# Optimization experiments

Measured on AMD Instinct MI355X. Metric: run time of the kernel, lower is better.

## Reference

```python
import jax, jax.numpy as jnp
import numpy as np

N_U, N_P, E = 200000, 50000, 500000
D_U, D_P, H, OUT = 100, 50, 128, 1
BN_EPS = 1e-5


def _lin(k, dout, din):
    s = 1.0 / np.sqrt(din)
    kw, kb = jax.random.split(k)
    W = jax.random.uniform(kw, (dout, din), jnp.float32, -s, s)
    b = jax.random.uniform(kb, (dout,), jnp.float32, -s, s)
    return W, b


def setup_inputs() -> dict:
    key = jax.random.key(0)
    ks = jax.random.split(key, 12)
    x_u = jax.random.normal(ks[0], (N_U, D_U), jnp.float32)
    x_p = jax.random.normal(ks[1], (N_P, D_P), jnp.float32)
    src = jax.random.randint(ks[2], (E,), 0, N_U, jnp.int64) if jax.config.jax_enable_x64 else jax.random.randint(ks[2], (E,), 0, N_U)
    dst = jax.random.randint(ks[3], (E,), N_U, N_U + N_P)
    edge_index = jnp.stack([src, dst]).astype(jnp.int32)
    W_u, b_u = _lin(ks[4], H, D_U)
    W_p, b_p = _lin(ks[5], H, D_P)
    W1l, b1l = _lin(ks[6], H, H)   # SAGEConv lin_l (aggregated neighbors, carries bias)
    W1r, _ = _lin(ks[7], H, H)     # SAGEConv lin_r (root, no bias)
    W2l, b2l = _lin(ks[8], H, H)
    W2r, _ = _lin(ks[9], H, H)
    W_out, b_out = _lin(ks[10], OUT, H)
    return dict(x_u=x_u, x_p=x_p, edge_index=edge_index,
                W_u=W_u, b_u=b_u, W_p=W_p, b_p=b_p,
                W1l=W1l, b1l=b1l, W1r=W1r,
                g1=jnp.ones((H,), jnp.float32), be1=jnp.zeros((H,), jnp.float32),
                W2l=W2l, b2l=b2l, W2r=W2r,
                g2=jnp.ones((H,), jnp.float32), be2=jnp.zeros((H,), jnp.float32),
                W_out=W_out, b_out=b_out)


def reference(x_u, x_p, edge_index, W_u, b_u, W_p, b_p,
              W1l, b1l, W1r, g1, be1, W2l, b2l, W2r, g2, be2,
              W_out, b_out):
    N = x_u.shape[0] + x_p.shape[0]
    # input projections + relu, then concat users/products -> [N, H]
    x = jnp.concatenate([jax.nn.relu(x_u @ W_u.T + b_u),
                         jax.nn.relu(x_p @ W_p.T + b_p)], axis=0)
    # to_undirected: add reversed edges (bipartite => no duplicates)
    src = jnp.concatenate([edge_index[0], edge_index[1]])
    dst = jnp.concatenate([edge_index[1], edge_index[0]])
    deg = jnp.maximum(jax.ops.segment_sum(jnp.ones_like(dst, jnp.float32), dst, num_segments=N), 1.0)

    def sage(h, Wl, bl, Wr):
        # mean aggregation of neighbor features, scatter by dst
        mean = jax.ops.segment_sum(h[src], dst, num_segments=N) / deg[:, None]
        return mean @ Wl.T + bl + h @ Wr.T

    def bn(h, g, b):
        m = h.mean(0)
        v = h.var(0)  # biased variance, as used for normalization in torch BN
        return (h - m) * jax.lax.rsqrt(v + BN_EPS) * g + b

    h1 = jax.nn.relu(bn(sage(x, W1l, b1l, W1r), g1, be1))   # dropout = identity (eval)
    h2 = jax.nn.relu(bn(sage(h1, W2l, b2l, W2r), g2, be2)) + x
    return h2[: x_u.shape[0]] @ W_out.T + b_out
```

## Files before the change

kernel.cpp:

```cpp
#include <hip/hip_runtime.h>
#include <hip/hip_bf16.h>
#include <cstdint>
#include <cstddef>

#define NT   250000
#define NUU  200000
#define NPP  50000
#define EG   500000
#define E2   1000000
#define HD   128
#define NBLK_SCAN 977

#define X_OFF     0ull
#define R1_OFF    64000000ull
#define R2_OFF    128000000ull
#define CNT_OFF   179200000ull
#define SPART_OFF 180200000ull
#define SS_OFF    180265536ull
#define RPTR_OFF  180267584ull
#define BSUM_OFF  181267588ull
#define BMAT_OFF  181271504ull
#define COL_OFF   181451728ull
#define WS_NEED   185451728ull

typedef __hip_bfloat16 bf16;
typedef __attribute__((ext_vector_type(8))) short short8v;
typedef __attribute__((ext_vector_type(4))) float f32x4;

__device__ inline float bflo(unsigned u) { return __builtin_bit_cast(float, u << 16); }
__device__ inline float bfhi(unsigned u) { return __builtin_bit_cast(float, u & 0xffff0000u); }
__device__ inline float b2f(short s) { return __builtin_bit_cast(float, ((unsigned)(unsigned short)s) << 16); }
__device__ inline unsigned short f2bf(float f) { return __builtin_bit_cast(unsigned short, __float2bfloat16(f)); }

__global__ __launch_bounds__(256) void k_zero(int* __restrict__ p, int n) {
    for (int i = blockIdx.x * 256 + threadIdx.x; i < n; i += gridDim.x * 256) p[i] = 0;
}

__global__ __launch_bounds__(256) void k_count(const int* __restrict__ ei, int* __restrict__ cnt) {
    for (int e = blockIdx.x * 256 + threadIdx.x; e < E2; e += gridDim.x * 256) {
        int d = (e < EG) ? ei[e + EG] : ei[e - EG];
        atomicAdd(&cnt[d], 1);
    }
}

__global__ __launch_bounds__(256) void k_scan1(const int* __restrict__ cnt, int* __restrict__ bsum) {
    __shared__ int lds[256];
    int i = blockIdx.x * 256 + threadIdx.x;
    int v = (i < NT) ? cnt[i] : 0;
    lds[threadIdx.x] = v; __syncthreads();
    for (int s = 128; s > 0; s >>= 1) {
        if (threadIdx.x < s) lds[threadIdx.x] += lds[threadIdx.x + s];
        __syncthreads();
    }
    if (threadIdx.x == 0) bsum[blockIdx.x] = lds[0];
}

__global__ __launch_bounds__(1024) void k_scan2(int* __restrict__ bsum) {
    __shared__ int lds[1024];
    int i = threadIdx.x;
    int v = (i < NBLK_SCAN) ? bsum[i] : 0;
    lds[i] = v; __syncthreads();
    for (int off = 1; off < 1024; off <<= 1) {
        int t = (i >= off) ? lds[i - off] : 0;
        __syncthreads();
        lds[i] += t;
        __syncthreads();
    }
    if (i < NBLK_SCAN) bsum[i] = lds[i] - v;
}

__global__ __launch_bounds__(256) void k_scan3(const int* __restrict__ cnt, const int* __restrict__ bsum,
                                               int* __restrict__ rp) {
    __shared__ int lds[256];
    int i = blockIdx.x * 256 + threadIdx.x;
    int v = (i < NT) ? cnt[i] : 0;
    lds[threadIdx.x] = v; __syncthreads();
    for (int off = 1; off < 256; off <<= 1) {
        int t = (threadIdx.x >= off) ? lds[threadIdx.x - off] : 0;
        __syncthreads();
        lds[threadIdx.x] += t;
        __syncthreads();
    }
    if (i < NT) rp[i] = bsum[blockIdx.x] + lds[threadIdx.x] - v;
    if (i == 0 && blockIdx.x == 0) rp[NT] = E2;
}

__global__ __launch_bounds__(256) void k_fill(const int* __restrict__ ei, const int* __restrict__ rp,
                                              int* __restrict__ fill, int* __restrict__ col) {
    for (int e = blockIdx.x * 256 + threadIdx.x; e < E2; e += gridDim.x * 256) {
        int s = ei[e];
        int d = (e < EG) ? ei[e + EG] : ei[e - EG];
        int slot = rp[d] + atomicAdd(&fill[d], 1);
        col[slot] = s;
    }
}

__global__ __launch_bounds__(256) void k_wcvt(const float* __restrict__ W1l, const float* __restrict__ W1r,
                                              const float* __restrict__ W2l, const float* __restrict__ W2r,
                                              const float* __restrict__ Wu, const float* __restrict__ Wp,
                                              bf16* __restrict__ B) {
    int i = blockIdx.x * 256 + threadIdx.x;
    if (i < 65536) {
        int layer = i >> 15, rem = i & 32767, o = rem >> 8, k = rem & 255;
        const float* W = layer ? ((k < 128) ? W2l : W2r) : ((k < 128) ? W1l : W1r);
        B[i] = __float2bfloat16(W[o * 128 + (k & 127)]);
    } else if (i < 81920) {
        int rem = i - 65536, o = rem >> 7, k = rem & 127;
        B[i] = __float2bfloat16((k < 100) ? Wu[o * 100 + k] : 0.f);
    } else if (i < 90112) {
        int rem = i - 81920, o = rem >> 6, k = rem & 63;
        B[i] = __float2bfloat16((k < 50) ? Wp[o * 50 + k] : 0.f);
    }
}

template<int DIN, int KPAD>
__global__ __launch_bounds__(256) void k_projm(const float* __restrict__ in, const bf16* __restrict__ Bp,
                                               const float* __restrict__ bias, bf16* __restrict__ outp,
                                               int nrows, int rowbase) {
    const int lane = threadIdx.x & 63;
    const int wid = threadIdx.x >> 6;
    const int wr = wid >> 1, wc = wid & 1;
    const int r15 = lane & 15, l4 = lane >> 4;
    const int tb = blockIdx.x * 128;
    constexpr int NKS = KPAD / 32;

    f32x4 acc[4][4] = {};
#pragma unroll
    for (int ks = 0; ks < NKS; ks++) {
        int kk = ks * 32 + l4 * 8;
        short8v a[4], b[4];
#pragma unroll
        for (int m = 0; m < 4; m++) {
            int r = tb + wr * 64 + m * 16 + r15;
            if (r > nrows - 1) r = nrows - 1;
            const float* src = in + (size_t)r * DIN + kk;
            short8v v;
            if constexpr (DIN >= 32 * (1) && true) {
                if (ks * 32 + 32 <= DIN) {
                    const float2* s2 = (const float2*)src;
                    float2 f0 = s2[0], f1 = s2[1], f2 = s2[2], f3 = s2[3];
                    v[0] = (short)f2bf(f0.x); v[1] = (short)f2bf(f0.y);
                    v[2] = (short)f2bf(f1.x); v[3] = (short)f2bf(f1.y);
                    v[4] = (short)f2bf(f2.x); v[5] = (short)f2bf(f2.y);
                    v[6] = (short)f2bf(f3.x); v[7] = (short)f2bf(f3.y);
                } else {
#pragma unroll
                    for (int j = 0; j < 8; j++) {
                        float f = (kk + j < DIN) ? src[j] : 0.f;
                        v[j] = (short)f2bf(f);
                    }
                }
            }
            a[m] = v;
        }
#pragma unroll
        for (int n = 0; n < 4; n++) {
            int c = wc * 64 + n * 16 + r15;
            b[n] = *(const short8v*)(Bp + (size_t)c * KPAD + kk);
        }
#pragma unroll
        for (int m = 0; m < 4; m++)
#pragma unroll
            for (int n = 0; n < 4; n++)
                acc[m][n] = __builtin_amdgcn_mfma_f32_16x16x32_bf16(a[m], b[n], acc[m][n], 0, 0, 0);
    }
    float bcol[4];
#pragma unroll
    for (int n = 0; n < 4; n++) bcol[n] = bias[wc * 64 + n * 16 + r15];
#pragma unroll
    for (int m = 0; m < 4; m++)
#pragma unroll
        for (int n = 0; n < 4; n++)
#pragma unroll
            for (int g = 0; g < 4; g++) {
                int row = tb + wr * 64 + m * 16 + l4 * 4 + g;
                if (row < nrows) {
                    float v = fmaxf(acc[m][n][g] + bcol[n], 0.f);
                    outp[(size_t)(rowbase + row) * HD + wc * 64 + n * 16 + r15] = __float2bfloat16(v);
                }
            }
}

template<bool NORM>
__global__ __launch_bounds__(256) void k_gemm(const bf16* __restrict__ hin, const float* __restrict__ ssv,
                                              const int* __restrict__ rp, const int* __restrict__ col,
                                              const bf16* __restrict__ Bmat, const float* __restrict__ blv,
                                              bf16* __restrict__ outp, float* __restrict__ spart,
                                              int store_n) {
    __shared__ unsigned int mrow[8192];
    const int tid = threadIdx.x;
    const int lane = tid & 63;
    const int wid = tid >> 6;
    const int g16 = lane >> 4, l16 = lane & 15;
    const int tb = blockIdx.x * 128;
    const int wnb = wid * 32;

    float sv[8], tv[8];
    if (NORM) {
        int f0 = l16 * 8;
#pragma unroll
        for (int j = 0; j < 8; j++) { sv[j] = ssv[f0 + j]; tv[j] = ssv[HD + f0 + j]; }
    }

    int rpv = 0;
    if (lane <= 32) {
        int idx = tb + wnb + lane;
        rpv = rp[min(idx, NT)];
    }

    for (int t = 0; t < 8; t++) {
        int nl = wnb + t * 4 + g16;
        int node = tb + nl;
        int s0 = __shfl(rpv, t * 4 + g16);
        int s1 = __shfl(rpv, t * 4 + g16 + 1);
        if (node >= NT) { s0 = 0; s1 = 0; }
        float a[8] = {0.f, 0.f, 0.f, 0.f, 0.f, 0.f, 0.f, 0.f};
        for (int p = s0; p < s1; p += 4) {
            int c0 = col[p];
            int c1 = col[min(p + 1, s1 - 1)];
            int c2 = col[min(p + 2, s1 - 1)];
            int c3 = col[min(p + 3, s1 - 1)];
            short8v u0 = *(const short8v*)(hin + (size_t)c0 * HD + l16 * 8);
            short8v u1 = *(const short8v*)(hin + (size_t)c1 * HD + l16 * 8);
            short8v u2 = *(const short8v*)(hin + (size_t)c2 * HD + l16 * 8);
            short8v u3 = *(const short8v*)(hin + (size_t)c3 * HD + l16 * 8);
            float m1 = (p + 1 < s1) ? 1.f : 0.f;
            float m2 = (p + 2 < s1) ? 1.f : 0.f;
            float m3 = (p + 3 < s1) ? 1.f : 0.f;
#pragma unroll
            for (int j = 0; j < 8; j++) {
                float v0 = b2f(u0[j]), v1 = b2f(u1[j]), v2 = b2f(u2[j]), v3 = b2f(u3[j]);
                if (NORM) {
                    v0 = fmaxf(fmaf(v0, sv[j], tv[j]), 0.f);
                    v1 = fmaxf(fmaf(v1, sv[j], tv[j]), 0.f);
                    v2 = fmaxf(fmaf(v2, sv[j], tv[j]), 0.f);
                    v3 = fmaxf(fmaf(v3, sv[j], tv[j]), 0.f);
                }
                a[j] += v0 + m1 * v1 + m2 * v2 + m3 * v3;
            }
        }
        float inv = 1.f / (float)max(s1 - s0, 1);
        short8v w;
#pragma unroll
        for (int j = 0; j < 8; j++) w[j] = (short)f2bf(a[j] * inv);
        int byte = (nl * 256 + l16 * 16) ^ ((nl & 7) << 4);
        *(short8v*)((char*)mrow + byte) = w;
    }
    __syncthreads();

    const int wr = wid >> 1, wc = wid & 1;
    const int r15 = lane & 15, l4 = lane >> 4;
    f32x4 acc[4][4] = {};
#pragma unroll
    for (int ks = 0; ks < 8; ks++) {
        short8v a[4], b[4];
        if (ks < 4) {
            int kb = ks * 64 + l4 * 16;
#pragma unroll
            for (int m = 0; m < 4; m++) {
                int r = wr * 64 + m * 16 + r15;
                int byte = (r * 256 + kb) ^ ((r & 7) << 4);
                a[m] = *(const short8v*)((const char*)mrow + byte);
            }
        } else {
            int k2 = (ks - 4) * 32 + l4 * 8;
            float sv2[8], tv2[8];
            if (NORM) {
#pragma unroll
                for (int j = 0; j < 8; j++) { sv2[j] = ssv[k2 + j]; tv2[j] = ssv[HD + k2 + j]; }
            }
#pragma unroll
            for (int m = 0; m < 4; m++) {
                int r = tb + wr * 64 + m * 16 + r15; if (r > NT - 1) r = NT - 1;
                short8v v = *(const short8v*)(hin + (size_t)r * HD + k2);
                if (NORM) {
#pragma unroll
                    for (int j = 0; j < 8; j++) {
                        float f = b2f(v[j]);
                        f = fmaxf(fmaf(f, sv2[j], tv2[j]), 0.f);
                        v[j] = (short)f2bf(f);
                    }
                }
                a[m] = v;
            }
        }
#pragma unroll
        for (int n = 0; n < 4; n++) {
            int c = wc * 64 + n * 16 + r15;
            b[n] = *(const short8v*)(Bmat + (size_t)c * 256 + ks * 32 + l4 * 8);
        }
#pragma unroll
        for (int m = 0; m < 4; m++)
#pragma unroll
            for (int n = 0; n < 4; n++)
                acc[m][n] = __builtin_amdgcn_mfma_f32_16x16x32_bf16(a[m], b[n], acc[m][n], 0, 0, 0);
    }

    float bcol[4];
#pragma unroll
    for (int n = 0; n < 4; n++) bcol[n] = blv[wc * 64 + n * 16 + r15];
    float ls[4] = {0.f, 0.f, 0.f, 0.f}, lq[4] = {0.f, 0.f, 0.f, 0.f};
#pragma unroll
    for (int m = 0; m < 4; m++)
#pragma unroll
        for (int n = 0; n < 4; n++)
#pragma unroll
            for (int g = 0; g < 4; g++) {
                int row = tb + wr * 64 + m * 16 + l4 * 4 + g;
                float v = acc[m][n][g] + bcol[n];
                if (row < NT) { ls[n] += v; lq[n] += v * v; }
                if (row < store_n)
                    outp[(size_t)row * HD + wc * 64 + n * 16 + r15] = __float2bfloat16(v);
            }
    int part = (blockIdx.x & 31) * 256;
#pragma unroll
    for (int n = 0; n < 4; n++) {
        float s = ls[n], q2 = lq[n];
        s  += __shfl_xor(s, 16);  s  += __shfl_xor(s, 32);
        q2 += __shfl_xor(q2, 16); q2 += __shfl_xor(q2, 32);
        if (l4 == 0) {
            int c = wc * 64 + n * 16 + r15;
            atomicAdd(&spart[part + c], s);
            atomicAdd(&spart[part + 128 + c], q2);
        }
    }
}

__global__ void k_fin(const float* __restrict__ sp, const float* __restrict__ g,
                      const float* __restrict__ be, float* __restrict__ ssout) {
    int j = threadIdx.x;
    float m = 0.f, q = 0.f;
    for (int i = 0; i < 32; i++) { m += sp[i * 256 + j]; q += sp[i * 256 + 128 + j]; }
    m *= (1.f / (float)NT);
    q = q * (1.f / (float)NT) - m * m;
    float s = g[j] * rsqrtf(q + 1e-5f);
    ssout[j] = s;
    ssout[HD + j] = be[j] - m * s;
}

__global__ __launch_bounds__(256) void k_out(const bf16* __restrict__ r2, const float* __restrict__ ss,
                                             const bf16* __restrict__ x, const float* __restrict__ wout,
                                             const float* __restrict__ bout, float* __restrict__ outp) {
    int lane = threadIdx.x & 63;
    int wid = (blockIdx.x * blockDim.x + threadIdx.x) >> 6;
    int nwv = (gridDim.x * blockDim.x) >> 6;
    int j0 = lane * 2;
    float s0 = ss[j0],       s1 = ss[j0 + 1];
    float t0 = ss[HD + j0],  t1 = ss[HD + j0 + 1];
    float w0 = wout[j0], w1 = wout[j0 + 1];
    float bo = bout[0];
    for (int r = wid; r < NUU; r += nwv) {
        unsigned ua = *(const unsigned*)(r2 + (size_t)r * HD + j0);
        unsigned ux = *(const unsigned*)(x + (size_t)r * HD + j0);
        float h0 = fmaxf(fmaf(bflo(ua), s0, t0), 0.f) + bflo(ux);
        float h1 = fmaxf(fmaf(bfhi(ua), s1, t1), 0.f) + bfhi(ux);
        float acc = h0 * w0 + h1 * w1;
#pragma unroll
        for (int off = 32; off; off >>= 1) acc += __shfl_down(acc, off);
        if (lane == 0) outp[r] = acc + bo;
    }
}

extern "C" void kernel_launch(void* const* d_in, const int* in_sizes, int n_in,
                              void* d_out, int out_size, void* d_ws, size_t ws_size,
                              hipStream_t stream) {
    const float* x_u = (const float*)d_in[0];
    const float* x_p = (const float*)d_in[1];
    const int*   ei  = (const int*)d_in[2];
    const float* W_u = (const float*)d_in[3];
    const float* b_u = (const float*)d_in[4];
    const float* W_p = (const float*)d_in[5];
    const float* b_p = (const float*)d_in[6];
    const float* W1l = (const float*)d_in[7];
    const float* b1l = (const float*)d_in[8];
    const float* W1r = (const float*)d_in[9];
    const float* g1  = (const float*)d_in[10];
    const float* be1 = (const float*)d_in[11];
    const float* W2l = (const float*)d_in[12];
    const float* b2l = (const float*)d_in[13];
    const float* W2r = (const float*)d_in[14];
    const float* g2  = (const float*)d_in[15];
    const float* be2 = (const float*)d_in[16];
    const float* Wout = (const float*)d_in[17];
    const float* bout = (const float*)d_in[18];

    float* out = (float*)d_out;

    if (ws_size < WS_NEED) {
        k_zero<<<512, 256, 0, stream>>>((int*)d_out, out_size);
        return;
    }

    char* ws = (char*)d_ws;
    bf16* X      = (bf16*)(ws + X_OFF);
    bf16* R1     = (bf16*)(ws + R1_OFF);
    bf16* R2     = (bf16*)(ws + R2_OFF);
    int*  cnt    = (int*)(ws + CNT_OFF);
    float* spart = (float*)(ws + SPART_OFF);
    float* ssbuf = (float*)(ws + SS_OFF);
    int*  rp     = (int*)(ws + RPTR_OFF);
    int*  bsum   = (int*)(ws + BSUM_OFF);
    bf16* Bmat   = (bf16*)(ws + BMAT_OFF);
    int*  col    = (int*)(ws + COL_OFF);

    k_zero<<<1043, 256, 0, stream>>>(cnt, 266896);
    k_wcvt<<<352, 256, 0, stream>>>(W1l, W1r, W2l, W2r, W_u, W_p, Bmat);

    k_count<<<1024, 256, 0, stream>>>(ei, cnt);
    k_scan1<<<NBLK_SCAN, 256, 0, stream>>>(cnt, bsum);
    k_scan2<<<1, 1024, 0, stream>>>(bsum);
    k_scan3<<<NBLK_SCAN, 256, 0, stream>>>(cnt, bsum, rp);
    k_zero<<<977, 256, 0, stream>>>(cnt, NT);
    k_fill<<<1024, 256, 0, stream>>>(ei, rp, cnt, col);

    k_projm<100, 128><<<1563, 256, 0, stream>>>(x_u, Bmat + 65536, b_u, X, NUU, 0);
    k_projm<50, 64><<<391, 256, 0, stream>>>(x_p, Bmat + 81920, b_p, X, NPP, NUU);

    k_gemm<false><<<1954, 256, 0, stream>>>(X, nullptr, rp, col, Bmat, b1l, R1, spart, NT);
    k_fin<<<1, 128, 0, stream>>>(spart, g1, be1, ssbuf);

    k_gemm<true><<<1954, 256, 0, stream>>>(R1, ssbuf, rp, col, Bmat + 32768, b2l, R2, spart + 8192, NUU);
    k_fin<<<1, 128, 0, stream>>>(spart + 8192, g2, be2, ssbuf + 256);

    k_out<<<2048, 256, 0, stream>>>(R2, ssbuf + 256, X, Wout, bout, out);
}
```

Measured before the change: 464.9 us.

## Interleave product tiles among user tiles and gather two nodes per iteration

```diff
diff --git a/kernel.cpp b/kernel.cpp
--- a/kernel.cpp
+++ b/kernel.cpp
@@ -10,6 +10,7 @@
 #define E2   1000000
 #define HD   128
 #define NBLK_SCAN 977
+#define NTILES 1954
 
 #define X_OFF     0ull
 #define R1_OFF    64000000ull
@@ -135,20 +136,18 @@
             if (r > nrows - 1) r = nrows - 1;
             const float* src = in + (size_t)r * DIN + kk;
             short8v v;
-            if constexpr (DIN >= 32 * (1) && true) {
-                if (ks * 32 + 32 <= DIN) {
-                    const float2* s2 = (const float2*)src;
-                    float2 f0 = s2[0], f1 = s2[1], f2 = s2[2], f3 = s2[3];
-                    v[0] = (short)f2bf(f0.x); v[1] = (short)f2bf(f0.y);
-                    v[2] = (short)f2bf(f1.x); v[3] = (short)f2bf(f1.y);
-                    v[4] = (short)f2bf(f2.x); v[5] = (short)f2bf(f2.y);
-                    v[6] = (short)f2bf(f3.x); v[7] = (short)f2bf(f3.y);
-                } else {
-#pragma unroll
-                    for (int j = 0; j < 8; j++) {
-                        float f = (kk + j < DIN) ? src[j] : 0.f;
-                        v[j] = (short)f2bf(f);
-                    }
+            if (ks * 32 + 32 <= DIN) {
+                const float2* s2 = (const float2*)src;
+                float2 f0 = s2[0], f1 = s2[1], f2 = s2[2], f3 = s2[3];
+                v[0] = (short)f2bf(f0.x); v[1] = (short)f2bf(f0.y);
+                v[2] = (short)f2bf(f1.x); v[3] = (short)f2bf(f1.y);
+                v[4] = (short)f2bf(f2.x); v[5] = (short)f2bf(f2.y);
+                v[6] = (short)f2bf(f3.x); v[7] = (short)f2bf(f3.y);
+            } else {
+#pragma unroll
+                for (int j = 0; j < 8; j++) {
+                    float f = (kk + j < DIN) ? src[j] : 0.f;
+                    v[j] = (short)f2bf(f);
                 }
             }
             a[m] = v;
@@ -187,64 +186,95 @@
                                               const bf16* __restrict__ Bmat, const float* __restrict__ blv,
                                               bf16* __restrict__ outp, float* __restrict__ spart,
                                               int store_n) {
+    int g = blockIdx.x / 5, pos = blockIdx.x % 5;
+    int tile = (pos < 4) ? (g * 4 + pos) : (1563 + g);
+    if (pos < 4 && tile > 1562) return;
+
     __shared__ unsigned int mrow[8192];
     const int tid = threadIdx.x;
     const int lane = tid & 63;
     const int wid = tid >> 6;
     const int g16 = lane >> 4, l16 = lane & 15;
-    const int tb = blockIdx.x * 128;
+    const int tb = tile * 128;
     const int wnb = wid * 32;
+    const int fo = l16 * 8;
 
     float sv[8], tv[8];
     if (NORM) {
-        int f0 = l16 * 8;
-#pragma unroll
-        for (int j = 0; j < 8; j++) { sv[j] = ssv[f0 + j]; tv[j] = ssv[HD + f0 + j]; }
+#pragma unroll
+        for (int j = 0; j < 8; j++) { sv[j] = ssv[fo + j]; tv[j] = ssv[HD + fo + j]; }
     }
 
     int rpv = 0;
-    if (lane <= 32) {
-        int idx = tb + wnb + lane;
-        rpv = rp[min(idx, NT)];
-    }
-
-    for (int t = 0; t < 8; t++) {
-        int nl = wnb + t * 4 + g16;
-        int node = tb + nl;
-        int s0 = __shfl(rpv, t * 4 + g16);
-        int s1 = __shfl(rpv, t * 4 + g16 + 1);
-        if (node >= NT) { s0 = 0; s1 = 0; }
-        float a[8] = {0.f, 0.f, 0.f, 0.f, 0.f, 0.f, 0.f, 0.f};
-        for (int p = s0; p < s1; p += 4) {
-            int c0 = col[p];
-            int c1 = col[min(p + 1, s1 - 1)];
-            int c2 = col[min(p + 2, s1 - 1)];
-            int c3 = col[min(p + 3, s1 - 1)];
-            short8v u0 = *(const short8v*)(hin + (size_t)c0 * HD + l16 * 8);
-            short8v u1 = *(const short8v*)(hin + (size_t)c1 * HD + l16 * 8);
-            short8v u2 = *(const short8v*)(hin + (size_t)c2 * HD + l16 * 8);
-            short8v u3 = *(const short8v*)(hin + (size_t)c3 * HD + l16 * 8);
-            float m1 = (p + 1 < s1) ? 1.f : 0.f;
-            float m2 = (p + 2 < s1) ? 1.f : 0.f;
-            float m3 = (p + 3 < s1) ? 1.f : 0.f;
+    if (lane <= 32) rpv = rp[min(tb + wnb + lane, NT)];
+
+    for (int t = 0; t < 4; t++) {
+        int nlA = wnb + t * 8 + g16;
+        int nlB = nlA + 4;
+        int a0 = __shfl(rpv, t * 8 + g16),     a1 = __shfl(rpv, t * 8 + g16 + 1);
+        int b0 = __shfl(rpv, t * 8 + g16 + 4), b1 = __shfl(rpv, t * 8 + g16 + 5);
+        if (tb + nlA >= NT) { a0 = 0; a1 = 0; }
+        if (tb + nlB >= NT) { b0 = 0; b1 = 0; }
+        float accA[8] = {}, accB[8] = {};
+        int pA = a0, pB = b0;
+        while (pA < a1 || pB < b1) {
+            int iA0 = (pA     < a1) ? pA     : 0;
+            int iA1 = (pA + 1 < a1) ? pA + 1 : 0;
+            int iA2 = (pA + 2 < a1) ? pA + 2 : 0;
+            int iA3 = (pA + 3 < a1) ? pA + 3 : 0;
+            int iB0 = (pB     < b1) ? pB     : 0;
+            int iB1 = (pB + 1 < b1) ? pB + 1 : 0;
+            int iB2 = (pB + 2 < b1) ? pB + 2 : 0;
+            int iB3 = (pB + 3 < b1) ? pB + 3 : 0;
+            int cA0 = col[iA0], cA1 = col[iA1], cA2 = col[iA2], cA3 = col[iA3];
+            int cB0 = col[iB0], cB1 = col[iB1], cB2 = col[iB2], cB3 = col[iB3];
+            short8v uA0 = *(const short8v*)(hin + (size_t)cA0 * HD + fo);
+            short8v uA1 = *(const short8v*)(hin + (size_t)cA1 * HD + fo);
+            short8v uA2 = *(const short8v*)(hin + (size_t)cA2 * HD + fo);
+            short8v uA3 = *(const short8v*)(hin + (size_t)cA3 * HD + fo);
+            short8v uB0 = *(const short8v*)(hin + (size_t)cB0 * HD + fo);
+            short8v uB1 = *(const short8v*)(hin + (size_t)cB1 * HD + fo);
+            short8v uB2 = *(const short8v*)(hin + (size_t)cB2 * HD + fo);
+            short8v uB3 = *(const short8v*)(hin + (size_t)cB3 * HD + fo);
+            float mA0 = (pA     < a1) ? 1.f : 0.f;
+            float mA1 = (pA + 1 < a1) ? 1.f : 0.f;
+            float mA2 = (pA + 2 < a1) ? 1.f : 0.f;
+            float mA3 = (pA + 3 < a1) ? 1.f : 0.f;
+            float mB0 = (pB     < b1) ? 1.f : 0.f;
+            float mB1 = (pB + 1 < b1) ? 1.f : 0.f;
+            float mB2 = (pB + 2 < b1) ? 1.f : 0.f;
+            float mB3 = (pB + 3 < b1) ? 1.f : 0.f;
 #pragma unroll
             for (int j = 0; j < 8; j++) {
-                float v0 = b2f(u0[j]), v1 = b2f(u1[j]), v2 = b2f(u2[j]), v3 = b2f(u3[j]);
+                float vA0 = b2f(uA0[j]), vA1 = b2f(uA1[j]), vA2 = b2f(uA2[j]), vA3 = b2f(uA3[j]);
+                float vB0 = b2f(uB0[j]), vB1 = b2f(uB1[j]), vB2 = b2f(uB2[j]), vB3 = b2f(uB3[j]);
                 if (NORM) {
-                    v0 = fmaxf(fmaf(v0, sv[j], tv[j]), 0.f);
-                    v1 = fmaxf(fmaf(v1, sv[j], tv[j]), 0.f);
-                    v2 = fmaxf(fmaf(v2, sv[j], tv[j]), 0.f);
-                    v3 = fmaxf(fmaf(v3, sv[j], tv[j]), 0.f);
+                    vA0 = fmaxf(fmaf(vA0, sv[j], tv[j]), 0.f);
+                    vA1 = fmaxf(fmaf(vA1, sv[j], tv[j]), 0.f);
+                    vA2 = fmaxf(fmaf(vA2, sv[j], tv[j]), 0.f);
+                    vA3 = fmaxf(fmaf(vA3, sv[j], tv[j]), 0.f);
+                    vB0 = fmaxf(fmaf(vB0, sv[j], tv[j]), 0.f);
+                    vB1 = fmaxf(fmaf(vB1, sv[j], tv[j]), 0.f);
+                    vB2 = fmaxf(fmaf(vB2, sv[j], tv[j]), 0.f);
+                    vB3 = fmaxf(fmaf(vB3, sv[j], tv[j]), 0.f);
                 }
-                a[j] += v0 + m1 * v1 + m2 * v2 + m3 * v3;
-            }
-        }
-        float inv = 1.f / (float)max(s1 - s0, 1);
-        short8v w;
-#pragma unroll
-        for (int j = 0; j < 8; j++) w[j] = (short)f2bf(a[j] * inv);
-        int byte = (nl * 256 + l16 * 16) ^ ((nl & 7) << 4);
-        *(short8v*)((char*)mrow + byte) = w;
+                accA[j] += mA0 * vA0 + mA1 * vA1 + mA2 * vA2 + mA3 * vA3;
+                accB[j] += mB0 * vB0 + mB1 * vB1 + mB2 * vB2 + mB3 * vB3;
+            }
+            pA += 4; pB += 4;
+        }
+        float invA = 1.f / (float)max(a1 - a0, 1);
+        float invB = 1.f / (float)max(b1 - b0, 1);
+        short8v wA, wB;
+#pragma unroll
+        for (int j = 0; j < 8; j++) {
+            wA[j] = (short)f2bf(accA[j] * invA);
+            wB[j] = (short)f2bf(accB[j] * invB);
+        }
+        int byteA = (nlA * 256 + l16 * 16) ^ ((nlA & 7) << 4);
+        int byteB = (nlB * 256 + l16 * 16) ^ ((nlB & 7) << 4);
+        *(short8v*)((char*)mrow + byteA) = wA;
+        *(short8v*)((char*)mrow + byteB) = wB;
     }
     __syncthreads();
 
@@ -305,14 +335,14 @@
 #pragma unroll
         for (int n = 0; n < 4; n++)
 #pragma unroll
-            for (int g = 0; g < 4; g++) {
-                int row = tb + wr * 64 + m * 16 + l4 * 4 + g;
-                float v = acc[m][n][g] + bcol[n];
+            for (int gg = 0; gg < 4; gg++) {
+                int row = tb + wr * 64 + m * 16 + l4 * 4 + gg;
+                float v = acc[m][n][gg] + bcol[n];
                 if (row < NT) { ls[n] += v; lq[n] += v * v; }
                 if (row < store_n)
                     outp[(size_t)row * HD + wc * 64 + n * 16 + r15] = __float2bfloat16(v);
             }
-    int part = (blockIdx.x & 31) * 256;
+    int part = (tile & 31) * 256;
 #pragma unroll
     for (int n = 0; n < 4; n++) {
         float s = ls[n], q2 = lq[n];
@@ -416,10 +446,10 @@
     k_projm<100, 128><<<1563, 256, 0, stream>>>(x_u, Bmat + 65536, b_u, X, NUU, 0);
     k_projm<50, 64><<<391, 256, 0, stream>>>(x_p, Bmat + 81920, b_p, X, NPP, NUU);
 
-    k_gemm<false><<<1954, 256, 0, stream>>>(X, nullptr, rp, col, Bmat, b1l, R1, spart, NT);
+    k_gemm<false><<<1955, 256, 0, stream>>>(X, nullptr, rp, col, Bmat, b1l, R1, spart, NT);
     k_fin<<<1, 128, 0, stream>>>(spart, g1, be1, ssbuf);
 
-    k_gemm<true><<<1954, 256, 0, stream>>>(R1, ssbuf, rp, col, Bmat + 32768, b2l, R2, spart + 8192, NUU);
+    k_gemm<true><<<1955, 256, 0, stream>>>(R1, ssbuf, rp, col, Bmat + 32768, b2l, R2, spart + 8192, NUU);
     k_fin<<<1, 128, 0, stream>>>(spart + 8192, g2, be2, ssbuf + 256);
 
     k_out<<<2048, 256, 0, stream>>>(R2, ssbuf + 256, X, Wout, bout, out);
```

Measured after the change: 452.6 us. -2.6%, faster.
